# Performance work log

Measured on AMD Instinct MI355X. Metric: run time of the kernel, lower is better.

The kernel has to match this reference:

```python
import jax, jax.numpy as jnp
import numpy as np
import math

N, C, T, V = 8, 256, 120, 25
W = 5          # window_size
PAD = 2        # (W + (W-1)*(dil-1) - 1)//2 with dil=1
H = 8          # num_heads
CO = 256       # out_channels
HD = CO // H   # head channels
EPS = 1e-5


def _bn(x, g, b, m, v):
    # eval-mode BatchNorm2d over channel axis 1; x: (N, C, T, V)
    inv = jax.lax.rsqrt(v + EPS)
    return (x - m[None, :, None, None]) * (inv * g)[None, :, None, None] + b[None, :, None, None]


def _mish(x):
    return x * jnp.tanh(jax.nn.softplus(x))


def setup_inputs() -> dict:
    key = jax.random.key(0)
    ks = jax.random.split(key, 16)
    s_in = 1.0 / math.sqrt(C)
    s_out = 1.0 / math.sqrt(CO)
    return {
        "x": jax.random.normal(ks[0], (N, C, T, V), jnp.float32),
        "w_qkv": jax.random.normal(ks[1], (C, 3 * CO), jnp.float32) * s_in,
        "w_out": jax.random.normal(ks[2], (CO, CO), jnp.float32) * s_out,
        "b_out": jax.random.normal(ks[3], (CO,), jnp.float32) * 0.01,
        "bn1_g": jax.random.normal(ks[4], (CO,), jnp.float32) * 0.1 + 1.0,
        "bn1_b": jax.random.normal(ks[5], (CO,), jnp.float32) * 0.1,
        "ffn_w1": jax.random.normal(ks[6], (CO, CO), jnp.float32) * s_out,
        "ffn_w2": jax.random.normal(ks[7], (CO, CO), jnp.float32) * s_out,
        "ffn_g": jax.random.normal(ks[8], (CO,), jnp.float32) * 0.1 + 1.0,
        "ffn_b": jax.random.normal(ks[9], (CO,), jnp.float32) * 0.1,
        "bn2_g": jax.random.normal(ks[10], (CO,), jnp.float32) * 0.1 + 1.0,
        "bn2_b": jax.random.normal(ks[11], (CO,), jnp.float32) * 0.1,
        "bn1_m": jax.random.normal(ks[12], (CO,), jnp.float32) * 0.1,
        "bn1_v": jax.random.uniform(ks[13], (CO,), jnp.float32, 0.5, 1.5),
        "ffn_m": jax.random.normal(ks[14], (CO,), jnp.float32) * 0.1,
        "ffn_v": jax.random.uniform(ks[15], (CO,), jnp.float32, 0.5, 1.5),
        "bn2_m": jnp.zeros((CO,), jnp.float32),
        "bn2_v": jnp.ones((CO,), jnp.float32),
    }


def reference(x, w_qkv, w_out, b_out, bn1_g, bn1_b, ffn_w1, ffn_w2, ffn_g, ffn_b,
              bn2_g, bn2_b, bn1_m, bn1_v, ffn_m, ffn_v, bn2_m, bn2_v):
    L = W * V
    # --- group_window: unfold over T with kernel (W,1), zero padding PAD ---
    xp = jnp.pad(x, ((0, 0), (0, 0), (PAD, PAD), (0, 0)))
    # (N, C, T, W, V): window element w at time t is frame t + w - PAD
    xw = jnp.stack([xp[:, :, w:w + T, :] for w in range(W)], axis=3)
    xg = xw.transpose(0, 2, 3, 4, 1).reshape(N * T, L, C)  # tokens: (N*T, L, C)

    # --- spatio-temporal attention (full softmax over L, scale 1/sqrt(CO)) ---
    qkv = (xg @ w_qkv).reshape(N * T, L, H, 3, HD)
    q, k, v = qkv[..., 0, :], qkv[..., 1, :], qkv[..., 2, :]  # (NT, L, H, HD)
    scores = jnp.einsum('blhd,bmhd->bhlm', q, k) / math.sqrt(CO)
    attn = jax.nn.softmax(scores, axis=-1)
    out = jnp.einsum('bhlm,bmhd->blhd', attn, v).reshape(N * T, L, CO)
    out = out @ w_out + b_out

    # --- mean over window dim, residual (Identity since C == CO), norm1 ---
    inter = out.reshape(N, T, W, V, CO).transpose(0, 4, 1, 2, 3).mean(axis=3)  # (N, CO, T, V)
    inter = _bn(inter + x, bn1_g, bn1_b, bn1_m, bn1_v)

    # --- FFN: 1x1 conv -> Mish -> BN -> 1x1 conv ---
    h = jnp.einsum('oi,nitv->notv', ffn_w1, inter)
    h = _bn(_mish(h), ffn_g, ffn_b, ffn_m, ffn_v)
    h = jnp.einsum('oi,nitv->notv', ffn_w2, h)

    return _bn(h + inter, bn2_g, bn2_b, bn2_m, bn2_v)
```

## Files before the change

kernel.cpp:

```cpp
#include <hip/hip_runtime.h>
#include <hip/hip_bf16.h>


using bf16  = __bf16;
using bf16x8 = __bf16 __attribute__((ext_vector_type(8)));
using f32x4  = float __attribute__((ext_vector_type(4)));
using f32x16 = float __attribute__((ext_vector_type(16)));
using uint32x4 = unsigned int __attribute__((ext_vector_type(4)));

#define GAS __attribute__((address_space(1)))
#define LAS __attribute__((address_space(3)))

__device__ __forceinline__ void gload_lds16(const void* g, void* l) {
  __builtin_amdgcn_global_load_lds((GAS void*)g, (LAS void*)l, 16, 0, 0);
}

__device__ __forceinline__ unsigned cvt_pk_bf16(float lo, float hi) {
  unsigned r;
  asm("v_cvt_pk_bf16_f32 %0, %1, %2" : "=v"(r) : "v"(lo), "v"(hi));
  return r;
}

__device__ __forceinline__ void pl32_swap(unsigned& a, unsigned& b) {
  asm("v_permlane32_swap_b32 %0, %1" : "+v"(a), "+v"(b));
}

__global__ void k_zero(float* out, int n) {
  int i = blockIdx.x * 256 + threadIdx.x;
  if (i < n) out[i] = 0.f;
}

__global__ void k_prep(const float* __restrict__ x,
                       const float* __restrict__ wqkv, const float* __restrict__ wout,
                       const float* __restrict__ b_out,
                       const float* __restrict__ w1, const float* __restrict__ w2,
                       const float* __restrict__ g1, const float* __restrict__ b1,
                       const float* __restrict__ m1, const float* __restrict__ v1,
                       const float* __restrict__ gf, const float* __restrict__ bff,
                       const float* __restrict__ mf, const float* __restrict__ vf,
                       const float* __restrict__ g2, const float* __restrict__ b2,
                       const float* __restrict__ m2, const float* __restrict__ v2,
                       bf16* __restrict__ Xrow, bf16* __restrict__ WqT,
                       bf16* __restrict__ WoT, bf16* __restrict__ W1c,
                       bf16* __restrict__ W2c, float* __restrict__ pb) {
  __shared__ bf16 T[64 * 72];
  const int b = blockIdx.x, tid = threadIdx.x;
  if (b < 1504) {
    const int bx = b % 47, by = (b / 47) & 3, n = b / 188;
    const int tv0 = bx * 64, c0 = by * 64;
    const int la = tid & 63, sub = tid >> 6;
#pragma unroll 4
    for (int i = 0; i < 16; ++i) {
      int c = c0 + sub + i * 4;
      int tv = tv0 + la;
      float v = (tv < 3000) ? x[(size_t)(n * 256 + c) * 3000 + tv] : 0.f;
      T[(sub + i * 4) * 72 + la] = (bf16)v;
    }
    __syncthreads();
#pragma unroll 4
    for (int i = 0; i < 16; ++i) {
      int tvl = sub + i * 4;
      int tv = tv0 + tvl;
      if (tv < 3000)
        Xrow[(size_t)(n * 3100 + 50 + tv) * 256 + c0 + la] = T[la * 72 + tvl];
    }
  } else if (b < 3041) {
    int idx = (b - 1504) * 256 + tid;
    if (idx < 196608) {
      int c = idx / 768, o = idx % 768;
      float vv = wqkv[idx];
      if ((o % 96) < 32) vv *= 0.0901387929f;
      WqT[o * 256 + c] = (bf16)vv;
    } else if (idx < 262144) {
      int j = idx - 196608;
      int c = j >> 8, o = j & 255;
      WoT[o * 256 + c] = (bf16)wout[j];
    } else if (idx < 327680) {
      int j = idx - 262144;
      W1c[j] = (bf16)w1[j];
    } else if (idx < 393216) {
      int j = idx - 327680;
      W2c[j] = (bf16)w2[j];
    } else if (idx < 393472) {
      int k = idx - 393216;
      float s1 = g1[k] * rsqrtf(v1[k] + 1e-5f);
      pb[k]        = s1;
      pb[256 + k]  = b1[k] - m1[k] * s1;
      float sf = gf[k] * rsqrtf(vf[k] + 1e-5f);
      pb[512 + k]  = sf;
      pb[768 + k]  = bff[k] - mf[k] * sf;
      float s2 = g2[k] * rsqrtf(v2[k] + 1e-5f);
      pb[1024 + k] = s2;
      pb[1280 + k] = b2[k] - m2[k] * s2;
      pb[1536 + k] = b_out[k];
    }
  } else {
    int z = b - 3041;
    int idx16 = z * 256 + tid;
    int e0 = idx16 * 8;
    int pr = e0 >> 8, col = e0 & 255;
    int n = pr / 100, r100 = pr % 100;
    int row = n * 3100 + (r100 < 50 ? r100 : 3000 + r100);
    int4 zz = {};
    *(int4*)&Xrow[(size_t)row * 256 + col] = zz;
  }
}

template <int EPI>
__global__ __launch_bounds__(256, 2) void k_gemm(
    const bf16* __restrict__ A, const bf16* __restrict__ BT,
    bf16* __restrict__ Cout, int ldc, int Mreal,
    const float* __restrict__ pb, const bf16* __restrict__ Res,
    float* __restrict__ Out2) {
  __shared__ __align__(16) char smem[19456];
  bf16* As = (bf16*)smem;
  bf16* Bs = (bf16*)(smem + 8192);
  const int tid = threadIdx.x;
  const int w = tid >> 6, lane = tid & 63, q = lane >> 4, l15 = lane & 15;
  const int m0 = blockIdx.x * 128, n0 = blockIdx.y * 128;
  const int wm = (w >> 1) * 64, wn = (w & 1) * 64;
  const int srow = tid >> 2;
  const int scol = (tid & 3) << 3;
  int ar1 = m0 + srow;        if (ar1 >= Mreal) ar1 = Mreal - 1;
  int ar2 = m0 + srow + 64;   if (ar2 >= Mreal) ar2 = Mreal - 1;
  char* ldsA = (char*)As + w * 1024;
  char* ldsB = (char*)Bs + w * 1024;
  f32x4 acc[4][4] = {};

  for (int ks = 0; ks < 8; ++ks) {
    const bf16* ga1 = A  + (size_t)ar1 * 256 + ks * 32 + scol;
    const bf16* ga2 = A  + (size_t)ar2 * 256 + ks * 32 + scol;
    const bf16* gb  = BT + (size_t)(n0 + srow) * 256 + ks * 32 + scol;
    gload_lds16(ga1, ldsA);
    gload_lds16(ga2, ldsA + 4096);
    gload_lds16(gb,            ldsB);
    gload_lds16(gb + 64 * 256, ldsB + 4096);
    __syncthreads();
    bf16x8 af[4], bfr[4];
#pragma unroll
    for (int i = 0; i < 4; ++i) af[i]  = *(const bf16x8*)&As[(wm + i * 16 + l15) * 32 + q * 8];
#pragma unroll
    for (int i = 0; i < 4; ++i) bfr[i] = *(const bf16x8*)&Bs[(wn + i * 16 + l15) * 32 + q * 8];
#pragma unroll
    for (int i = 0; i < 4; ++i)
#pragma unroll
      for (int j = 0; j < 4; ++j)
        acc[i][j] = __builtin_amdgcn_mfma_f32_16x16x32_bf16(af[i], bfr[j], acc[i][j], 0, 0, 0);
    __syncthreads();
  }

  if constexpr (EPI != 3) {
#pragma unroll
    for (int i = 0; i < 4; ++i) {
#pragma unroll
      for (int j = 0; j < 4; ++j) {
#pragma unroll
        for (int r = 0; r < 4; ++r) {
          int row = m0 + wm + i * 16 + q * 4 + r;
          int col = n0 + wn + j * 16 + l15;
          if (row >= Mreal) continue;
          float v = acc[i][j][r];
          if constexpr (EPI == 0) {
            Cout[(size_t)row * ldc + col] = (bf16)v;
          } else if constexpr (EPI == 1) {
            v += pb[1536 + col];
            int n = row / 3000;
            v += (float)Res[(size_t)(row + n * 100 + 50) * 256 + col];
            v = v * pb[col] + pb[256 + col];
            Cout[(size_t)row * 256 + col] = (bf16)v;
          } else {
            float ex = __expf(v);
            float a = 1.f + ex;
            float u = 1.f / (a * a);
            v = v * (1.f - u) / (1.f + u);
            v = v * pb[512 + col] + pb[768 + col];
            Cout[(size_t)row * 256 + col] = (bf16)v;
          }
        }
      }
    }
  } else {
    float* Tt = (float*)smem;
    const int tti = (w & 1);
#pragma unroll
    for (int jj = 0; jj < 4; ++jj) {
      __syncthreads();
#pragma unroll
      for (int i = 0; i < 4; ++i) {
#pragma unroll
        for (int r = 0; r < 4; ++r) {
          int rowl = wm + i * 16 + q * 4 + r;
          int row = m0 + rowl;
          int col = n0 + tti * 64 + jj * 16 + l15;
          float v = acc[i][jj][r];
          v += (float)Res[(size_t)row * 256 + col];
          v = v * pb[1024 + col] + pb[1280 + col];
          Tt[tti * 2432 + rowl * 19 + l15] = v;
        }
      }
      __syncthreads();
#pragma unroll
      for (int k = 0; k < 16; ++k) {
        int flat = k * 256 + tid;
        int tt2 = flat >> 11;
        int rem = flat & 2047;
        int colL = rem >> 7;
        int rowl = rem & 127;
        int row = m0 + rowl;
        if (row < Mreal) {
          int col = n0 + tt2 * 64 + jj * 16 + colL;
          int n = row / 3000, r2 = row - n * 3000;
          Out2[(size_t)(n * 256 + col) * 3000 + r2] = Tt[tt2 * 2432 + rowl * 19 + colL];
        }
      }
    }
  }
}

__global__ __launch_bounds__(256, 3) void k_ffn(
    const bf16* __restrict__ Aom, const bf16* __restrict__ Wo,
    const bf16* __restrict__ W1, const bf16* __restrict__ W2,
    const bf16* __restrict__ Xres, const float* __restrict__ pb,
    float* __restrict__ Out2) {
  __shared__ __align__(16) char smem[54272];
  bf16* As = (bf16*)smem;
  bf16* Bs = (bf16*)(smem + 4096);
  bf16* XI = (bf16*)(smem + 20480);
  float* Tt = (float*)smem;
  const int tid = threadIdx.x;
  const int w = tid >> 6, lane = tid & 63, q = lane >> 4, l15 = lane & 15;
  const int r0 = blockIdx.x * 64;
  const int srow = tid >> 2, scol = (tid & 3) << 3;
  char* ldsA = (char*)As + w * 1024;
  char* ldsB = (char*)Bs + w * 1024;

  f32x4 acc[4][4];
#pragma unroll
  for (int i = 0; i < 4; ++i)
#pragma unroll
    for (int j = 0; j < 4; ++j) acc[i][j] = f32x4{};

  for (int ks = 0; ks < 8; ++ks) {
    gload_lds16(Aom + (size_t)(r0 + srow) * 256 + ks * 32 + scol, ldsA);
#pragma unroll
    for (int ii = 0; ii < 4; ++ii)
      gload_lds16(Wo + (size_t)(ii * 64 + srow) * 256 + ks * 32 + scol,
                  ldsB + ii * 4096);
    __syncthreads();
    bf16x8 af[4], bfr[4];
#pragma unroll
    for (int i = 0; i < 4; ++i) af[i]  = *(const bf16x8*)&As[(i * 16 + l15) * 32 + q * 8];
#pragma unroll
    for (int j = 0; j < 4; ++j) bfr[j] = *(const bf16x8*)&Bs[(w * 64 + j * 16 + l15) * 32 + q * 8];
#pragma unroll
    for (int i = 0; i < 4; ++i)
#pragma unroll
      for (int j = 0; j < 4; ++j)
        acc[i][j] = __builtin_amdgcn_mfma_f32_16x16x32_bf16(af[i], bfr[j], acc[i][j], 0, 0, 0);
    __syncthreads();
  }
  unsigned irk[32];
#pragma unroll
  for (int i = 0; i < 4; ++i) {
#pragma unroll
    for (int j = 0; j < 4; ++j) {
      int colb = w * 64 + j * 16 + l15;
      float vv[4];
#pragma unroll
      for (int r = 0; r < 4; ++r) {
        int grow = r0 + i * 16 + q * 4 + r;
        int nn = grow / 3000;
        float v = acc[i][j][r] + pb[1536 + colb]
                + (float)Xres[(size_t)(grow + nn * 100 + 50) * 256 + colb];
        v = v * pb[colb] + pb[256 + colb];
        vv[r] = v;
        XI[(i * 16 + q * 4 + r) * 264 + colb] = (bf16)v;
      }
      irk[(i * 4 + j) * 2 + 0] = cvt_pk_bf16(vv[0], vv[1]);
      irk[(i * 4 + j) * 2 + 1] = cvt_pk_bf16(vv[2], vv[3]);
    }
  }

#pragma unroll
  for (int i = 0; i < 4; ++i)
#pragma unroll
    for (int j = 0; j < 4; ++j) acc[i][j] = f32x4{};
  for (int ks = 0; ks < 8; ++ks) {
#pragma unroll
    for (int ii = 0; ii < 4; ++ii)
      gload_lds16(W1 + (size_t)(ii * 64 + srow) * 256 + ks * 32 + scol,
                  ldsB + ii * 4096);
    __syncthreads();
    bf16x8 af[4], bfr[4];
#pragma unroll
    for (int i = 0; i < 4; ++i) af[i]  = *(const bf16x8*)&XI[(i * 16 + l15) * 264 + ks * 32 + q * 8];
#pragma unroll
    for (int j = 0; j < 4; ++j) bfr[j] = *(const bf16x8*)&Bs[(w * 64 + j * 16 + l15) * 32 + q * 8];
#pragma unroll
    for (int i = 0; i < 4; ++i)
#pragma unroll
      for (int j = 0; j < 4; ++j)
        acc[i][j] = __builtin_amdgcn_mfma_f32_16x16x32_bf16(af[i], bfr[j], acc[i][j], 0, 0, 0);
    __syncthreads();
  }
#pragma unroll
  for (int i = 0; i < 4; ++i) {
#pragma unroll
    for (int j = 0; j < 4; ++j) {
      int colb = w * 64 + j * 16 + l15;
#pragma unroll
      for (int r = 0; r < 4; ++r) {
        float v = acc[i][j][r];
        float ex = __expf(v);
        float a = 1.f + ex;
        float u = 1.f / (a * a);
        v = v * (1.f - u) / (1.f + u);
        v = v * pb[512 + colb] + pb[768 + colb];
        XI[(i * 16 + q * 4 + r) * 264 + colb] = (bf16)v;
      }
    }
  }

#pragma unroll
  for (int i = 0; i < 4; ++i)
#pragma unroll
    for (int j = 0; j < 4; ++j) acc[i][j] = f32x4{};
  for (int ks = 0; ks < 8; ++ks) {
#pragma unroll
    for (int ii = 0; ii < 4; ++ii)
      gload_lds16(W2 + (size_t)(ii * 64 + srow) * 256 + ks * 32 + scol,
                  ldsB + ii * 4096);
    __syncthreads();
    bf16x8 af[4], bfr[4];
#pragma unroll
    for (int i = 0; i < 4; ++i) af[i]  = *(const bf16x8*)&XI[(i * 16 + l15) * 264 + ks * 32 + q * 8];
#pragma unroll
    for (int j = 0; j < 4; ++j) bfr[j] = *(const bf16x8*)&Bs[(w * 64 + j * 16 + l15) * 32 + q * 8];
#pragma unroll
    for (int i = 0; i < 4; ++i)
#pragma unroll
      for (int j = 0; j < 4; ++j)
        acc[i][j] = __builtin_amdgcn_mfma_f32_16x16x32_bf16(af[i], bfr[j], acc[i][j], 0, 0, 0);
    __syncthreads();
  }

  const int rowl_t = tid & 63;
  const int grow_t = r0 + rowl_t;
  const int nn_t = grow_t / 3000;
  const int rr_t = grow_t - nn_t * 3000;
#pragma unroll
  for (int cc = 0; cc < 4; ++cc) {
    __syncthreads();
    if (w == cc) {
#pragma unroll
      for (int i = 0; i < 4; ++i) {
#pragma unroll
        for (int j = 0; j < 4; ++j) {
          int colb = cc * 64 + j * 16 + l15;
#pragma unroll
          for (int r = 0; r < 4; ++r) {
            unsigned pr = irk[(i * 4 + j) * 2 + (r >> 1)];
            unsigned short us = (r & 1) ? (unsigned short)(pr >> 16)
                                        : (unsigned short)(pr & 0xffff);
            float res = (float)__builtin_bit_cast(bf16, us);
            float v = acc[i][j][r] + res;
            v = v * pb[1024 + colb] + pb[1280 + colb];
            Tt[(i * 16 + q * 4 + r) * 65 + j * 16 + l15] = v;
          }
        }
      }
    }
    __syncthreads();
#pragma unroll
    for (int it = 0; it < 16; ++it) {
      int cl = (tid >> 6) + it * 4;
      int colb = cc * 64 + cl;
      Out2[(size_t)(nn_t * 256 + colb) * 3000 + rr_t] = Tt[rowl_t * 65 + cl];
    }
  }
}

__global__ __launch_bounds__(256, 4) void k_attn(const bf16* __restrict__ Y,
                                                 bf16* __restrict__ om) {
  __shared__ __align__(16) char smem[18944];
  bf16* Vts = (bf16*)smem;
  float* Ofl = (float*)smem;
  float* Rin = (float*)(smem + 18432);
  const int tid = threadIdx.x;
  const int bi = blockIdx.x;
  const int h = bi & 7, b = bi >> 3;
  const int n = b / 120, t = b % 120;
  const bf16* Yb = Y + (size_t)(n * 3100 + t * 25) * 768 + h * 96;
  const int w = tid >> 6, lane = tid & 63;
  const int l31 = lane & 31, hi = lane >> 5;

#pragma unroll
  for (int p = 0; p < 2; ++p) {
    int m = p * 64 + lane;
    if (m < 125) {
      int4 v4 = *(const int4*)(Yb + (size_t)m * 768 + 64 + w * 8);
      bf16x8 v8 = __builtin_bit_cast(bf16x8, v4);
#pragma unroll
      for (int jj = 0; jj < 8; ++jj) Vts[(w * 8 + jj) * 136 + m] = v8[jj];
    }
  }
  if (tid < 96) {
    int d = tid / 3, m = 125 + tid % 3;
    Vts[d * 136 + m] = (bf16)0.f;
  }

  int qrow = w * 32 + l31; if (qrow > 124) qrow = 124;
  const bf16* qp = Yb + (size_t)qrow * 768 + hi * 8;
  bf16x8 qf0 = *(const bf16x8*)qp;
  bf16x8 qf1 = *(const bf16x8*)(qp + 16);

  f32x16 acc[4] = {};
#pragma unroll
  for (int kt = 0; kt < 4; ++kt) {
    int krow = kt * 32 + l31; if (krow > 124) krow = 124;
    const bf16* kp = Yb + (size_t)krow * 768 + 32 + hi * 8;
    bf16x8 kf0 = *(const bf16x8*)kp;
    bf16x8 kf1 = *(const bf16x8*)(kp + 16);
    acc[kt] = __builtin_amdgcn_mfma_f32_32x32x16_bf16(kf0, qf0, acc[kt], 0, 0, 0);
    acc[kt] = __builtin_amdgcn_mfma_f32_32x32x16_bf16(kf1, qf1, acc[kt], 0, 0, 0);
  }

  float sp[4];
  uint32x4 pk[8];
#pragma unroll
  for (int kt = 0; kt < 4; ++kt) {
    float e[16];
#pragma unroll
    for (int r = 0; r < 16; ++r) {
      float pz = exp2f(acc[kt][r]);
      if (kt == 3 && r >= 13 && hi) pz = 0.f;
      e[r] = pz;
    }
    float t0 = (e[0] + e[1]) + (e[2] + e[3]);
    float t1 = (e[4] + e[5]) + (e[6] + e[7]);
    float t2 = (e[8] + e[9]) + (e[10] + e[11]);
    float t3 = (e[12] + e[13]) + (e[14] + e[15]);
    sp[kt] = (t0 + t1) + (t2 + t3);
#pragma unroll
    for (int half = 0; half < 2; ++half) {
      const int ba = half * 8;
      unsigned a0 = cvt_pk_bf16(e[ba + 0], e[ba + 1]);
      unsigned a1 = cvt_pk_bf16(e[ba + 2], e[ba + 3]);
      unsigned b0 = cvt_pk_bf16(e[ba + 4], e[ba + 5]);
      unsigned b1 = cvt_pk_bf16(e[ba + 6], e[ba + 7]);
      pl32_swap(a0, b0);
      pl32_swap(a1, b1);
      pk[kt * 2 + half][0] = a0;
      pk[kt * 2 + half][1] = a1;
      pk[kt * 2 + half][2] = b0;
      pk[kt * 2 + half][3] = b1;
    }
  }
  float s = (sp[0] + sp[1]) + (sp[2] + sp[3]);
  s += __shfl_xor(s, 32, 64);
  float rinv = 1.f / s;
  if (hi == 0) Rin[w * 32 + l31] = rinv;

  __syncthreads();

  f32x16 oacc0 = {}, oacc1 = {};
#pragma unroll
  for (int kc = 0; kc < 8; ++kc) {
    bf16x8 pa = __builtin_bit_cast(bf16x8, pk[kc]);
    bf16x8 vf = *(const bf16x8*)&Vts[l31 * 136 + kc * 16 + hi * 8];
    if (kc & 1) oacc1 = __builtin_amdgcn_mfma_f32_32x32x16_bf16(pa, vf, oacc1, 0, 0, 0);
    else        oacc0 = __builtin_amdgcn_mfma_f32_32x32x16_bf16(pa, vf, oacc0, 0, 0, 0);
  }

  __syncthreads();
#pragma unroll
  for (int r = 0; r < 16; ++r) {
    int row = w * 32 + (r & 3) + 8 * (r >> 2) + 4 * hi;
    Ofl[row * 36 + l31] = oacc0[r] + oacc1[r];
  }
  __syncthreads();
  bf16* dst = om + (size_t)((n * 120 + t) * 25) * 256 + h * 32;
  for (int j = tid; j < 800; j += 256) {
    int vv = j >> 5, d = j & 31;
    float s5 = 0.f;
#pragma unroll
    for (int ww = 0; ww < 5; ++ww)
      s5 += Ofl[(ww * 25 + vv) * 36 + d] * Rin[ww * 25 + vv];
    dst[vv * 256 + d] = (bf16)(s5 * 0.2f);
  }
}

extern "C" void kernel_launch(void* const* d_in, const int* in_sizes, int n_in,
                              void* d_out, int out_size, void* d_ws, size_t ws_size,
                              hipStream_t stream) {
  const size_t NEED1 = 51584000;
  const size_t NEED2 = 63872000;
  if (ws_size < NEED1) {
    k_zero<<<(out_size + 255) / 256, 256, 0, stream>>>((float*)d_out, out_size);
    return;
  }
  const float* x     = (const float*)d_in[0];
  const float* wqkv  = (const float*)d_in[1];
  const float* wout  = (const float*)d_in[2];
  const float* b_out = (const float*)d_in[3];
  const float* bn1_g = (const float*)d_in[4];
  const float* bn1_b = (const float*)d_in[5];
  const float* ffn_w1= (const float*)d_in[6];
  const float* ffn_w2= (const float*)d_in[7];
  const float* ffn_g = (const float*)d_in[8];
  const float* ffn_b = (const float*)d_in[9];
  const float* bn2_g = (const float*)d_in[10];
  const float* bn2_b = (const float*)d_in[11];
  const float* bn1_m = (const float*)d_in[12];
  const float* bn1_v = (const float*)d_in[13];
  const float* ffn_m = (const float*)d_in[14];
  const float* ffn_v = (const float*)d_in[15];
  const float* bn2_m = (const float*)d_in[16];
  const float* bn2_v = (const float*)d_in[17];

  char* ws = (char*)d_ws;
  float* pb    = (float*)(ws + 0);
  bf16* WqT    = (bf16*)(ws + 7168);
  bf16* WoT    = (bf16*)(ws + 400384);
  bf16* W1c    = (bf16*)(ws + 531456);
  bf16* W2c    = (bf16*)(ws + 662528);
  bf16* Xrow   = (bf16*)(ws + 793600);
  bf16* Y      = (bf16*)(ws + 13491200);
  bf16* interR = Y;
  bf16* Gm     = (bf16*)(ws + 25779200);
  bf16* om2    = (bf16*)(ws + 51584000);
  bf16* om     = (bf16*)d_out;

  k_prep<<<3141, 256, 0, stream>>>(x, wqkv, wout, b_out, ffn_w1, ffn_w2,
                                   bn1_g, bn1_b, bn1_m, bn1_v,
                                   ffn_g, ffn_b, ffn_m, ffn_v,
                                   bn2_g, bn2_b, bn2_m, bn2_v,
                                   Xrow, WqT, WoT, W1c, W2c, pb);
  k_gemm<0><<<dim3(194, 6), 256, 0, stream>>>(Xrow, WqT, Y, 768, 24800, pb, nullptr, nullptr);
  if (ws_size >= NEED2) {
    k_attn<<<7680, 256, 0, stream>>>(Y, om2);
    k_ffn<<<375, 256, 0, stream>>>(om2, WoT, W1c, W2c, Xrow, pb, (float*)d_out);
  } else {
    k_attn<<<7680, 256, 0, stream>>>(Y, om);
    k_gemm<1><<<dim3(188, 2), 256, 0, stream>>>(om, WoT, interR, 256, 24000, pb, Xrow, nullptr);
    k_gemm<2><<<dim3(188, 2), 256, 0, stream>>>(interR, W1c, Gm, 256, 24000, pb, nullptr, nullptr);
    k_gemm<3><<<dim3(188, 2), 256, 0, stream>>>(Gm, W2c, nullptr, 256, 24000, pb, interR, (float*)d_out);
  }
}
```

Measured before the change: 237.2 us.

## Double-buffer LDS tiles in GEMM and fused FFN kernels to overlap loads

Adds ping-pong LDS buffers to the generic GEMM and the fused FFN kernel. The next K-slice is prefetched with global_load_lds while the current slice feeds MFMAs, which removes one barrier per iteration. The first weight tile of each following FFN GEMM is prefetched during the previous epilogue. The cost is more LDS per block: the FFN kernel's launch bounds drop from 3 to 2 blocks per CU, so occupancy falls.

Result: faster. 214.5 us (-9.6%).

```diff
diff --git a/kernel.cpp b/kernel.cpp
--- a/kernel.cpp
+++ b/kernel.cpp
@@ -112,9 +112,7 @@
     bf16* __restrict__ Cout, int ldc, int Mreal,
     const float* __restrict__ pb, const bf16* __restrict__ Res,
     float* __restrict__ Out2) {
-  __shared__ __align__(16) char smem[19456];
-  bf16* As = (bf16*)smem;
-  bf16* Bs = (bf16*)(smem + 8192);
+  __shared__ __align__(16) char smem[32768];
   const int tid = threadIdx.x;
   const int w = tid >> 6, lane = tid & 63, q = lane >> 4, l15 = lane & 15;
   const int m0 = blockIdx.x * 128, n0 = blockIdx.y * 128;
@@ -123,30 +121,40 @@
   const int scol = (tid & 3) << 3;
   int ar1 = m0 + srow;        if (ar1 >= Mreal) ar1 = Mreal - 1;
   int ar2 = m0 + srow + 64;   if (ar2 >= Mreal) ar2 = Mreal - 1;
-  char* ldsA = (char*)As + w * 1024;
-  char* ldsB = (char*)Bs + w * 1024;
+  const bf16* gA1 = A  + (size_t)ar1 * 256 + scol;
+  const bf16* gA2 = A  + (size_t)ar2 * 256 + scol;
+  const bf16* gB1 = BT + (size_t)(n0 + srow) * 256 + scol;
+  const bf16* gB2 = gB1 + 64 * 256;
   f32x4 acc[4][4] = {};
 
+  auto STAGE = [&](int ks, char* buf) {
+    char* ldsA = buf + w * 1024;
+    char* ldsB = buf + 8192 + w * 1024;
+    gload_lds16(gA1 + ks * 32, ldsA);
+    gload_lds16(gA2 + ks * 32, ldsA + 4096);
+    gload_lds16(gB1 + ks * 32, ldsB);
+    gload_lds16(gB2 + ks * 32, ldsB + 4096);
+  };
+
+  int cur = 0;
+  STAGE(0, smem);
+  __syncthreads();
   for (int ks = 0; ks < 8; ++ks) {
-    const bf16* ga1 = A  + (size_t)ar1 * 256 + ks * 32 + scol;
-    const bf16* ga2 = A  + (size_t)ar2 * 256 + ks * 32 + scol;
-    const bf16* gb  = BT + (size_t)(n0 + srow) * 256 + ks * 32 + scol;
-    gload_lds16(ga1, ldsA);
-    gload_lds16(ga2, ldsA + 4096);
-    gload_lds16(gb,            ldsB);
-    gload_lds16(gb + 64 * 256, ldsB + 4096);
-    __syncthreads();
+    if (ks < 7) STAGE(ks + 1, smem + ((cur ^ 1) << 14));
+    const bf16* Asc = (const bf16*)(smem + (cur << 14));
+    const bf16* Bsc = Asc + 4096;
     bf16x8 af[4], bfr[4];
 #pragma unroll
-    for (int i = 0; i < 4; ++i) af[i]  = *(const bf16x8*)&As[(wm + i * 16 + l15) * 32 + q * 8];
-#pragma unroll
-    for (int i = 0; i < 4; ++i) bfr[i] = *(const bf16x8*)&Bs[(wn + i * 16 + l15) * 32 + q * 8];
+    for (int i = 0; i < 4; ++i) af[i]  = *(const bf16x8*)&Asc[(wm + i * 16 + l15) * 32 + q * 8];
+#pragma unroll
+    for (int i = 0; i < 4; ++i) bfr[i] = *(const bf16x8*)&Bsc[(wn + i * 16 + l15) * 32 + q * 8];
 #pragma unroll
     for (int i = 0; i < 4; ++i)
 #pragma unroll
       for (int j = 0; j < 4; ++j)
         acc[i][j] = __builtin_amdgcn_mfma_f32_16x16x32_bf16(af[i], bfr[j], acc[i][j], 0, 0, 0);
     __syncthreads();
+    cur ^= 1;
   }
 
   if constexpr (EPI != 3) {
@@ -217,22 +225,30 @@
   }
 }
 
-__global__ __launch_bounds__(256, 3) void k_ffn(
+__global__ __launch_bounds__(256, 2) void k_ffn(
     const bf16* __restrict__ Aom, const bf16* __restrict__ Wo,
     const bf16* __restrict__ W1, const bf16* __restrict__ W2,
     const bf16* __restrict__ Xres, const float* __restrict__ pb,
     float* __restrict__ Out2) {
-  __shared__ __align__(16) char smem[54272];
-  bf16* As = (bf16*)smem;
-  bf16* Bs = (bf16*)(smem + 4096);
-  bf16* XI = (bf16*)(smem + 20480);
+  __shared__ __align__(16) char smem[74752];
+  bf16* XI = (bf16*)(smem + 40960);
   float* Tt = (float*)smem;
   const int tid = threadIdx.x;
   const int w = tid >> 6, lane = tid & 63, q = lane >> 4, l15 = lane & 15;
   const int r0 = blockIdx.x * 64;
   const int srow = tid >> 2, scol = (tid & 3) << 3;
-  char* ldsA = (char*)As + w * 1024;
-  char* ldsB = (char*)Bs + w * 1024;
+
+  auto STAGE_A = [&](int ks, int b) {
+    gload_lds16(Aom + (size_t)(r0 + srow) * 256 + ks * 32 + scol,
+                smem + (b << 12) + w * 1024);
+  };
+  auto STAGE_B = [&](const bf16* Wsrc, int ks, int b) {
+    char* ldsB = smem + 8192 + (b << 14) + w * 1024;
+#pragma unroll
+    for (int ii = 0; ii < 4; ++ii)
+      gload_lds16(Wsrc + (size_t)(ii * 64 + srow) * 256 + ks * 32 + scol,
+                  ldsB + ii * 4096);
+  };
 
   f32x4 acc[4][4];
 #pragma unroll
@@ -240,25 +256,27 @@
 #pragma unroll
     for (int j = 0; j < 4; ++j) acc[i][j] = f32x4{};
 
+  int cur = 0;
+  STAGE_A(0, 0); STAGE_B(Wo, 0, 0);
+  __syncthreads();
   for (int ks = 0; ks < 8; ++ks) {
-    gload_lds16(Aom + (size_t)(r0 + srow) * 256 + ks * 32 + scol, ldsA);
-#pragma unroll
-    for (int ii = 0; ii < 4; ++ii)
-      gload_lds16(Wo + (size_t)(ii * 64 + srow) * 256 + ks * 32 + scol,
-                  ldsB + ii * 4096);
-    __syncthreads();
+    if (ks < 7) { STAGE_A(ks + 1, cur ^ 1); STAGE_B(Wo, ks + 1, cur ^ 1); }
+    const bf16* Asc = (const bf16*)(smem + (cur << 12));
+    const bf16* Bsc = (const bf16*)(smem + 8192 + (cur << 14));
     bf16x8 af[4], bfr[4];
 #pragma unroll
-    for (int i = 0; i < 4; ++i) af[i]  = *(const bf16x8*)&As[(i * 16 + l15) * 32 + q * 8];
-#pragma unroll
-    for (int j = 0; j < 4; ++j) bfr[j] = *(const bf16x8*)&Bs[(w * 64 + j * 16 + l15) * 32 + q * 8];
+    for (int i = 0; i < 4; ++i) af[i]  = *(const bf16x8*)&Asc[(i * 16 + l15) * 32 + q * 8];
+#pragma unroll
+    for (int j = 0; j < 4; ++j) bfr[j] = *(const bf16x8*)&Bsc[(w * 64 + j * 16 + l15) * 32 + q * 8];
 #pragma unroll
     for (int i = 0; i < 4; ++i)
 #pragma unroll
       for (int j = 0; j < 4; ++j)
         acc[i][j] = __builtin_amdgcn_mfma_f32_16x16x32_bf16(af[i], bfr[j], acc[i][j], 0, 0, 0);
     __syncthreads();
-  }
+    cur ^= 1;
+  }
+  STAGE_B(W1, 0, 0);
   unsigned irk[32];
 #pragma unroll
   for (int i = 0; i < 4; ++i) {
@@ -280,29 +298,30 @@
       irk[(i * 4 + j) * 2 + 1] = cvt_pk_bf16(vv[2], vv[3]);
     }
   }
+  __syncthreads();
 
 #pragma unroll
   for (int i = 0; i < 4; ++i)
 #pragma unroll
     for (int j = 0; j < 4; ++j) acc[i][j] = f32x4{};
+  cur = 0;
   for (int ks = 0; ks < 8; ++ks) {
-#pragma unroll
-    for (int ii = 0; ii < 4; ++ii)
-      gload_lds16(W1 + (size_t)(ii * 64 + srow) * 256 + ks * 32 + scol,
-                  ldsB + ii * 4096);
-    __syncthreads();
+    if (ks < 7) STAGE_B(W1, ks + 1, cur ^ 1);
+    const bf16* Bsc = (const bf16*)(smem + 8192 + (cur << 14));
     bf16x8 af[4], bfr[4];
 #pragma unroll
     for (int i = 0; i < 4; ++i) af[i]  = *(const bf16x8*)&XI[(i * 16 + l15) * 264 + ks * 32 + q * 8];
 #pragma unroll
-    for (int j = 0; j < 4; ++j) bfr[j] = *(const bf16x8*)&Bs[(w * 64 + j * 16 + l15) * 32 + q * 8];
+    for (int j = 0; j < 4; ++j) bfr[j] = *(const bf16x8*)&Bsc[(w * 64 + j * 16 + l15) * 32 + q * 8];
 #pragma unroll
     for (int i = 0; i < 4; ++i)
 #pragma unroll
       for (int j = 0; j < 4; ++j)
         acc[i][j] = __builtin_amdgcn_mfma_f32_16x16x32_bf16(af[i], bfr[j], acc[i][j], 0, 0, 0);
     __syncthreads();
-  }
+    cur ^= 1;
+  }
+  STAGE_B(W2, 0, 0);
 #pragma unroll
   for (int i = 0; i < 4; ++i) {
 #pragma unroll
@@ -320,28 +339,28 @@
       }
     }
   }
+  __syncthreads();
 
 #pragma unroll
   for (int i = 0; i < 4; ++i)
 #pragma unroll
     for (int j = 0; j < 4; ++j) acc[i][j] = f32x4{};
+  cur = 0;
   for (int ks = 0; ks < 8; ++ks) {
-#pragma unroll
-    for (int ii = 0; ii < 4; ++ii)
-      gload_lds16(W2 + (size_t)(ii * 64 + srow) * 256 + ks * 32 + scol,
-                  ldsB + ii * 4096);
-    __syncthreads();
+    if (ks < 7) STAGE_B(W2, ks + 1, cur ^ 1);
+    const bf16* Bsc = (const bf16*)(smem + 8192 + (cur << 14));
     bf16x8 af[4], bfr[4];
 #pragma unroll
     for (int i = 0; i < 4; ++i) af[i]  = *(const bf16x8*)&XI[(i * 16 + l15) * 264 + ks * 32 + q * 8];
 #pragma unroll
-    for (int j = 0; j < 4; ++j) bfr[j] = *(const bf16x8*)&Bs[(w * 64 + j * 16 + l15) * 32 + q * 8];
+    for (int j = 0; j < 4; ++j) bfr[j] = *(const bf16x8*)&Bsc[(w * 64 + j * 16 + l15) * 32 + q * 8];
 #pragma unroll
     for (int i = 0; i < 4; ++i)
 #pragma unroll
       for (int j = 0; j < 4; ++j)
         acc[i][j] = __builtin_amdgcn_mfma_f32_16x16x32_bf16(af[i], bfr[j], acc[i][j], 0, 0, 0);
     __syncthreads();
+    cur ^= 1;
   }
 
   const int rowl_t = tid & 63;
```
